# Performance work log

Measured on AMD Instinct MI355X. Metric: run time of the kernel, lower is better.

The kernel has to match this reference:

```python
import jax, jax.numpy as jnp
import numpy as np

N = 50000   # nodes
E = 800000  # edges
K = 3       # hops per TAGConv


def _row_normalize(x):
    row_sum = jnp.clip(jnp.sum(x, axis=1, keepdims=True), 1e-8, None)
    return x / row_sum


def _gcn_norm(edge_index, num_nodes):
    # PyG gcn_norm with add_self_loops=False (TAGConv default), edge_weight=1
    src, dst = edge_index[0], edge_index[1]
    deg = jax.ops.segment_sum(jnp.ones((src.shape[0],), jnp.float32), dst,
                              num_segments=num_nodes)
    deg_inv_sqrt = jnp.where(deg > 0, jnp.where(deg > 0, deg, 1.0) ** -0.5, 0.0)
    return deg_inv_sqrt[src] * deg_inv_sqrt[dst]  # [E]


def _propagate(x, src, dst, norm, num_nodes):
    # out[dst] += norm * x[src]   (sparse sym-normalized SpMM)
    return jax.ops.segment_sum(norm[:, None] * x[src], dst, num_segments=num_nodes)


def _tagconv(x, edge_index, norm, W, b):
    # W: [K+1, d_in, d_out]; out = sum_k A_hat^k x @ W_k + b
    src, dst = edge_index[0], edge_index[1]
    n = x.shape[0]
    hops = [x]
    for _ in range(W.shape[0] - 1):
        hops.append(_propagate(hops[-1], src, dst, norm, n))
    H = jnp.stack(hops)  # [K+1, N, d_in]
    return jnp.einsum('knd,kdo->no', H, W) + b


def setup_inputs() -> dict:
    key = jax.random.key(0)
    k1, k2, k3, k4 = jax.random.split(key, 4)
    x = jax.random.normal(k1, (N, 128), jnp.float32)
    edge_index = jax.random.randint(k2, (2, E), 0, N, jnp.int32)
    W1 = jax.random.normal(k3, (K + 1, 128, 16), jnp.float32) * 0.1
    b1 = jnp.zeros((16,), jnp.float32)
    W2 = jax.random.normal(k4, (K + 1, 16, 64), jnp.float32) * 0.1
    b2 = jnp.zeros((64,), jnp.float32)
    return {"x": x, "edge_index": edge_index, "W1": W1, "b1": b1,
            "W2": W2, "b2": b2}


def reference(x, edge_index, W1, b1, W2, b2):
    n = x.shape[0]
    norm = _gcn_norm(edge_index, n)
    h = _row_normalize(x)
    h = jax.nn.relu(_tagconv(h, edge_index, norm, W1, b1))
    # dropout is identity in eval mode
    return _tagconv(h, edge_index, norm, W2, b2)
```

## Files before the change

kernel.cpp:

```cpp
#include <hip/hip_runtime.h>
#include <hip/hip_bf16.h>

typedef unsigned short u16;

__device__ __forceinline__ float bf2f(u16 h) {
    return __uint_as_float(((unsigned int)h) << 16);
}
__device__ __forceinline__ u16 f2bf(float f) {
    __hip_bfloat16 h = __float2bfloat16(f);
    return *reinterpret_cast<u16*>(&h);
}

__global__ void pos_kernel(const int* __restrict__ dst, int* __restrict__ cnt,
                           int* __restrict__ pos, int E) {
    int e = blockIdx.x * blockDim.x + threadIdx.x;
    if (e < E) pos[e] = atomicAdd(&cnt[dst[e]], 1);
}

__global__ __launch_bounds__(256) void scanA_kernel(const int* __restrict__ cnt,
                                                    int* __restrict__ rowptr,
                                                    int* __restrict__ bsum, int n) {
    __shared__ int lds[256];
    int i = blockIdx.x * 256 + threadIdx.x;
    int v = (i < n) ? cnt[i] : 0;
    lds[threadIdx.x] = v;
    __syncthreads();
    #pragma unroll
    for (int off = 1; off < 256; off <<= 1) {
        int t = (threadIdx.x >= off) ? lds[threadIdx.x - off] : 0;
        __syncthreads();
        lds[threadIdx.x] += t;
        __syncthreads();
    }
    if (i < n) rowptr[i + 1] = lds[threadIdx.x];
    if (threadIdx.x == 255) bsum[blockIdx.x] = lds[255];
}

__global__ __launch_bounds__(1024) void scanB_kernel(int* __restrict__ bsum, int nb) {
    __shared__ int lds[1024];
    int t = threadIdx.x;
    int v = (t < nb) ? bsum[t] : 0;
    lds[t] = v;
    __syncthreads();
    #pragma unroll
    for (int off = 1; off < 1024; off <<= 1) {
        int u = (t >= off) ? lds[t - off] : 0;
        __syncthreads();
        lds[t] += u;
        __syncthreads();
    }
    if (t < nb) bsum[t] = lds[t] - v;
}

__global__ __launch_bounds__(256) void scanC_dis_kernel(int* __restrict__ rowptr,
                                                        const int* __restrict__ bsum,
                                                        const int* __restrict__ cnt,
                                                        float* __restrict__ dis, int n) {
    int i = blockIdx.x * 256 + threadIdx.x;
    if (i < n) {
        rowptr[i + 1] += bsum[blockIdx.x];
        int d = cnt[i];
        dis[i] = (d > 0) ? rsqrtf((float)d) : 0.0f;
    }
    if (i == 0) rowptr[0] = 0;
}

__global__ __launch_bounds__(1024) void scan_kernel(const int* __restrict__ cnt,
                                                    int* __restrict__ rowptr, int n) {
    __shared__ int part[1024];
    int tid = threadIdx.x;
    int chunk = (n + 1023) / 1024;
    int beg = tid * chunk;
    int end = beg + chunk; if (end > n) end = n;
    int s = 0;
    for (int i = beg; i < end; ++i) s += cnt[i];
    part[tid] = s;
    __syncthreads();
    for (int off = 1; off < 1024; off <<= 1) {
        int v = (tid >= off) ? part[tid - off] : 0;
        __syncthreads();
        part[tid] += v;
        __syncthreads();
    }
    int run = (tid > 0) ? part[tid - 1] : 0;
    if (tid == 0) rowptr[0] = 0;
    for (int i = beg; i < end; ++i) { run += cnt[i]; rowptr[i + 1] = run; }
}

__global__ void dis_only_kernel(const int* __restrict__ cnt, float* __restrict__ dis, int n) {
    int i = blockIdx.x * blockDim.x + threadIdx.x;
    if (i < n) {
        int d = cnt[i];
        dis[i] = (d > 0) ? rsqrtf((float)d) : 0.0f;
    }
}

__global__ void scatter2_kernel(const int* __restrict__ src, const int* __restrict__ dst,
                                const int* __restrict__ pos, const float* __restrict__ dis,
                                const int* __restrict__ rowptr,
                                float2* __restrict__ ecolw, int E) {
    int e = blockIdx.x * blockDim.x + threadIdx.x;
    if (e < E) {
        int s = src[e], d = dst[e];
        ecolw[rowptr[d] + pos[e]] = make_float2(__int_as_float(s), dis[s] * dis[d]);
    }
}

__global__ __launch_bounds__(256) void gemm1_bf_kernel(
    const float* __restrict__ x, const float* __restrict__ W1,
    u16* __restrict__ zb, int n, int nstride)
{
    __shared__ float As[64 * 132];
    __shared__ float Bs[64 * 64];
    __shared__ float sums[128];
    const int t  = threadIdx.x;
    const int tx = t & 15;
    const int ty = t >> 4;
    const int c  = t & 15;
    const int g  = t >> 4;
    const int block_row = blockIdx.x * 128;

    float acc[8][4];
    #pragma unroll
    for (int i = 0; i < 8; ++i)
        #pragma unroll
        for (int j = 0; j < 4; ++j) acc[i][j] = 0.f;

    for (int kp = 0; kp < 2; ++kp) {
        #pragma unroll
        for (int i = 0; i < 8; ++i) {
            int row  = g + 16 * i;
            int grow = block_row + row;
            float v0 = 0.f, v1 = 0.f, v2 = 0.f, v3 = 0.f;
            if (grow < n) {
                const float* xp = x + (long)grow * 128 + kp * 64 + c;
                v0 = xp[0]; v1 = xp[16]; v2 = xp[32]; v3 = xp[48];
            }
            As[(c +  0) * 132 + row] = v0;
            As[(c + 16) * 132 + row] = v1;
            As[(c + 32) * 132 + row] = v2;
            As[(c + 48) * 132 + row] = v3;
            float red = (v0 + v1) + (v2 + v3);
            #pragma unroll
            for (int off = 8; off > 0; off >>= 1) red += __shfl_down(red, off, 16);
            if (c == 0) { if (kp == 0) sums[row] = red; else sums[row] += red; }
        }
        #pragma unroll
        for (int i2 = 0; i2 < 4; ++i2) {
            int kk = g + 16 * i2;
            int kglob = kp * 64 + kk;
            float4 wv = *(const float4*)(W1 + (c >> 2) * 2048 + kglob * 16 + 4 * (c & 3));
            *(float4*)(Bs + kk * 64 + 4 * c) = wv;
        }
        __syncthreads();
        #pragma unroll 4
        for (int kk = 0; kk < 64; ++kk) {
            float4 a0 = *(const float4*)(As + kk * 132 + 8 * ty);
            float4 a1 = *(const float4*)(As + kk * 132 + 8 * ty + 4);
            float4 bv = *(const float4*)(Bs + kk * 64 + 4 * tx);
            float ar[8] = {a0.x, a0.y, a0.z, a0.w, a1.x, a1.y, a1.z, a1.w};
            float br[4] = {bv.x, bv.y, bv.z, bv.w};
            #pragma unroll
            for (int i = 0; i < 8; ++i)
                #pragma unroll
                for (int j = 0; j < 4; ++j)
                    acc[i][j] += ar[i] * br[j];
        }
        __syncthreads();
    }
    int plane = tx >> 2;
    int oo4   = 4 * (tx & 3);
    #pragma unroll
    for (int i = 0; i < 8; ++i) {
        int row  = 8 * ty + i;
        int grow = block_row + row;
        if (grow < n) {
            float s = 1.0f / fmaxf(sums[row], 1e-8f);
            ushort4 o;
            o.x = f2bf(acc[i][0] * s); o.y = f2bf(acc[i][1] * s);
            o.z = f2bf(acc[i][2] * s); o.w = f2bf(acc[i][3] * s);
            *(ushort4*)(zb + (long)plane * nstride + (long)grow * 16 + oo4) = o;
        }
    }
}

__global__ __launch_bounds__(256) void spmm_csr_bf_kernel(
    const u16* __restrict__ in, const u16* __restrict__ addsrc,
    u16* __restrict__ out, const int* __restrict__ rowptr,
    const float2* __restrict__ ecolw, const float* __restrict__ b,
    int relu, int n)
{
    int t = blockIdx.x * blockDim.x + threadIdx.x;
    int r = t >> 2, q = t & 3;
    if (r >= n) return;
    int e0 = rowptr[r], e1 = rowptr[r + 1];
    float a0x=0,a0y=0,a0z=0,a0w=0, a1x=0,a1y=0,a1z=0,a1w=0;
    float a2x=0,a2y=0,a2z=0,a2w=0, a3x=0,a3y=0,a3z=0,a3w=0;
    int e = e0;
    for (; e + 4 <= e1; e += 4) {
        float2 c0 = ecolw[e], c1 = ecolw[e+1], c2 = ecolw[e+2], c3 = ecolw[e+3];
        ushort4 v0 = *((const ushort4*)(in + (long)__float_as_int(c0.x) * 16) + q);
        ushort4 v1 = *((const ushort4*)(in + (long)__float_as_int(c1.x) * 16) + q);
        ushort4 v2 = *((const ushort4*)(in + (long)__float_as_int(c2.x) * 16) + q);
        ushort4 v3 = *((const ushort4*)(in + (long)__float_as_int(c3.x) * 16) + q);
        a0x += c0.y * bf2f(v0.x); a0y += c0.y * bf2f(v0.y); a0z += c0.y * bf2f(v0.z); a0w += c0.y * bf2f(v0.w);
        a1x += c1.y * bf2f(v1.x); a1y += c1.y * bf2f(v1.y); a1z += c1.y * bf2f(v1.z); a1w += c1.y * bf2f(v1.w);
        a2x += c2.y * bf2f(v2.x); a2y += c2.y * bf2f(v2.y); a2z += c2.y * bf2f(v2.z); a2w += c2.y * bf2f(v2.w);
        a3x += c3.y * bf2f(v3.x); a3y += c3.y * bf2f(v3.y); a3z += c3.y * bf2f(v3.z); a3w += c3.y * bf2f(v3.w);
    }
    for (; e < e1; ++e) {
        float2 c0 = ecolw[e];
        ushort4 v0 = *((const ushort4*)(in + (long)__float_as_int(c0.x) * 16) + q);
        a0x += c0.y * bf2f(v0.x); a0y += c0.y * bf2f(v0.y); a0z += c0.y * bf2f(v0.z); a0w += c0.y * bf2f(v0.w);
    }
    float Ax = (a0x+a1x)+(a2x+a3x), Ay = (a0y+a1y)+(a2y+a3y);
    float Az = (a0z+a1z)+(a2z+a3z), Aw = (a0w+a1w)+(a2w+a3w);
    if (addsrc) {
        ushort4 s = *((const ushort4*)(addsrc + (long)r * 16) + q);
        Ax += bf2f(s.x); Ay += bf2f(s.y); Az += bf2f(s.z); Aw += bf2f(s.w);
    }
    if (b) {
        float4 bb = *((const float4*)b + q);
        Ax += bb.x; Ay += bb.y; Az += bb.z; Aw += bb.w;
    }
    if (relu) {
        Ax = fmaxf(Ax, 0.f); Ay = fmaxf(Ay, 0.f);
        Az = fmaxf(Az, 0.f); Aw = fmaxf(Aw, 0.f);
    }
    ushort4 o; o.x = f2bf(Ax); o.y = f2bf(Ay); o.z = f2bf(Az); o.w = f2bf(Aw);
    *((ushort4*)(out + (long)r * 16) + q) = o;
}

__global__ __launch_bounds__(256) void gemm2_bf_kernel(
    const u16* __restrict__ zb, const float* __restrict__ W2,
    const float* __restrict__ b2, float* __restrict__ out, int n, int nstride)
{
    __shared__ float As[64 * 132];
    __shared__ float Bs[64 * 64];
    const int t  = threadIdx.x;
    const int tx = t & 15;
    const int ty = t >> 4;
    const int c  = t & 15;
    const int g  = t >> 4;
    const int block_row = blockIdx.x * 128;

    float acc[8][4];
    #pragma unroll
    for (int i = 0; i < 8; ++i)
        #pragma unroll
        for (int j = 0; j < 4; ++j) acc[i][j] = 0.f;

    #pragma unroll
    for (int i = 0; i < 8; ++i) {
        int row  = g + 16 * i;
        int grow = block_row + row;
        float v0 = 0.f, v1 = 0.f, v2 = 0.f, v3 = 0.f;
        if (grow < n) {
            const u16* zp = zb + (long)grow * 16 + c;
            v0 = bf2f(zp[0]);
            v1 = bf2f(zp[(long)nstride]);
            v2 = bf2f(zp[2 * (long)nstride]);
            v3 = bf2f(zp[3 * (long)nstride]);
        }
        As[(c +  0) * 132 + row] = v0;
        As[(c + 16) * 132 + row] = v1;
        As[(c + 32) * 132 + row] = v2;
        As[(c + 48) * 132 + row] = v3;
    }
    #pragma unroll
    for (int i2 = 0; i2 < 4; ++i2) {
        int j = g + 16 * i2;
        float4 wv = *(const float4*)(W2 + j * 64 + 4 * c);
        *(float4*)(Bs + j * 64 + 4 * c) = wv;
    }
    __syncthreads();
    #pragma unroll 4
    for (int kk = 0; kk < 64; ++kk) {
        float4 a0 = *(const float4*)(As + kk * 132 + 8 * ty);
        float4 a1 = *(const float4*)(As + kk * 132 + 8 * ty + 4);
        float4 bv = *(const float4*)(Bs + kk * 64 + 4 * tx);
        float ar[8] = {a0.x, a0.y, a0.z, a0.w, a1.x, a1.y, a1.z, a1.w};
        float br[4] = {bv.x, bv.y, bv.z, bv.w};
        #pragma unroll
        for (int i = 0; i < 8; ++i)
            #pragma unroll
            for (int j = 0; j < 4; ++j)
                acc[i][j] += ar[i] * br[j];
    }
    float4 bias = *(const float4*)(b2 + 4 * tx);
    #pragma unroll
    for (int i = 0; i < 8; ++i) {
        int grow = block_row + 8 * ty + i;
        if (grow < n) {
            float4 o = make_float4(acc[i][0] + bias.x, acc[i][1] + bias.y,
                                   acc[i][2] + bias.z, acc[i][3] + bias.w);
            *(float4*)(out + (long)grow * 64 + 4 * tx) = o;
        }
    }
}

__global__ void deg_kernel(const int* __restrict__ dst, float* __restrict__ deg, int E) {
    int e = blockIdx.x * blockDim.x + threadIdx.x;
    if (e < E) atomicAdd(&deg[dst[e]], 1.0f);
}
__global__ void disf_kernel(float* __restrict__ deg, int n) {
    int i = blockIdx.x * blockDim.x + threadIdx.x;
    if (i < n) {
        float d = deg[i];
        deg[i] = (d > 0.0f) ? rsqrtf(d) : 0.0f;
    }
}
__global__ __launch_bounds__(256) void gemm1_f32_kernel(
    const float* __restrict__ x, const float* __restrict__ W1,
    float* __restrict__ z, int n, int nstride)
{
    __shared__ float As[64 * 132];
    __shared__ float Bs[64 * 64];
    __shared__ float sums[128];
    const int t  = threadIdx.x;
    const int tx = t & 15;
    const int ty = t >> 4;
    const int c  = t & 15;
    const int g  = t >> 4;
    const int block_row = blockIdx.x * 128;
    float acc[8][4];
    #pragma unroll
    for (int i = 0; i < 8; ++i)
        #pragma unroll
        for (int j = 0; j < 4; ++j) acc[i][j] = 0.f;
    for (int kp = 0; kp < 2; ++kp) {
        #pragma unroll
        for (int i = 0; i < 8; ++i) {
            int row  = g + 16 * i;
            int grow = block_row + row;
            float v0 = 0.f, v1 = 0.f, v2 = 0.f, v3 = 0.f;
            if (grow < n) {
                const float* xp = x + (long)grow * 128 + kp * 64 + c;
                v0 = xp[0]; v1 = xp[16]; v2 = xp[32]; v3 = xp[48];
            }
            As[(c +  0) * 132 + row] = v0;
            As[(c + 16) * 132 + row] = v1;
            As[(c + 32) * 132 + row] = v2;
            As[(c + 48) * 132 + row] = v3;
            float red = (v0 + v1) + (v2 + v3);
            #pragma unroll
            for (int off = 8; off > 0; off >>= 1) red += __shfl_down(red, off, 16);
            if (c == 0) { if (kp == 0) sums[row] = red; else sums[row] += red; }
        }
        #pragma unroll
        for (int i2 = 0; i2 < 4; ++i2) {
            int kk = g + 16 * i2;
            int kglob = kp * 64 + kk;
            float4 wv = *(const float4*)(W1 + (c >> 2) * 2048 + kglob * 16 + 4 * (c & 3));
            *(float4*)(Bs + kk * 64 + 4 * c) = wv;
        }
        __syncthreads();
        #pragma unroll 4
        for (int kk = 0; kk < 64; ++kk) {
            float4 a0 = *(const float4*)(As + kk * 132 + 8 * ty);
            float4 a1 = *(const float4*)(As + kk * 132 + 8 * ty + 4);
            float4 bv = *(const float4*)(Bs + kk * 64 + 4 * tx);
            float ar[8] = {a0.x, a0.y, a0.z, a0.w, a1.x, a1.y, a1.z, a1.w};
            float br[4] = {bv.x, bv.y, bv.z, bv.w};
            #pragma unroll
            for (int i = 0; i < 8; ++i)
                #pragma unroll
                for (int j = 0; j < 4; ++j)
                    acc[i][j] += ar[i] * br[j];
        }
        __syncthreads();
    }
    int plane = tx >> 2;
    int oo4   = 4 * (tx & 3);
    #pragma unroll
    for (int i = 0; i < 8; ++i) {
        int row  = 8 * ty + i;
        int grow = block_row + row;
        if (grow < n) {
            float s = 1.0f / fmaxf(sums[row], 1e-8f);
            float4 o = make_float4(acc[i][0] * s, acc[i][1] * s, acc[i][2] * s, acc[i][3] * s);
            *(float4*)(z + (long)plane * nstride + (long)grow * 16 + oo4) = o;
        }
    }
}
__global__ __launch_bounds__(256) void spmm_atomic_kernel(
    const float* __restrict__ in, float* __restrict__ out,
    const int* __restrict__ src, const int* __restrict__ dst,
    const float* __restrict__ dis, int E)
{
    int t = blockIdx.x * blockDim.x + threadIdx.x;
    int e = t >> 4, f = t & 15;
    if (e < E) {
        int s = src[e], d = dst[e];
        atomicAdd(&out[d * 16 + f], dis[s] * dis[d] * in[s * 16 + f]);
    }
}
__global__ void bias_relu_kernel(float* __restrict__ z0, const float* __restrict__ b, int total) {
    int i = blockIdx.x * blockDim.x + threadIdx.x;
    if (i < total) {
        float v = z0[i] + b[i & 15];
        z0[i] = v > 0.0f ? v : 0.0f;
    }
}
__global__ __launch_bounds__(256) void gemm2_f32_kernel(
    const float* __restrict__ z, const float* __restrict__ W2,
    const float* __restrict__ b2, float* __restrict__ out, int n, int nstride)
{
    __shared__ float As[64 * 132];
    __shared__ float Bs[64 * 64];
    const int t  = threadIdx.x;
    const int tx = t & 15;
    const int ty = t >> 4;
    const int c  = t & 15;
    const int g  = t >> 4;
    const int block_row = blockIdx.x * 128;
    float acc[8][4];
    #pragma unroll
    for (int i = 0; i < 8; ++i)
        #pragma unroll
        for (int j = 0; j < 4; ++j) acc[i][j] = 0.f;
    #pragma unroll
    for (int i = 0; i < 8; ++i) {
        int row  = g + 16 * i;
        int grow = block_row + row;
        float v0 = 0.f, v1 = 0.f, v2 = 0.f, v3 = 0.f;
        if (grow < n) {
            const float* zp = z + (long)grow * 16 + c;
            v0 = zp[0];
            v1 = zp[(long)nstride];
            v2 = zp[2 * (long)nstride];
            v3 = zp[3 * (long)nstride];
        }
        As[(c +  0) * 132 + row] = v0;
        As[(c + 16) * 132 + row] = v1;
        As[(c + 32) * 132 + row] = v2;
        As[(c + 48) * 132 + row] = v3;
    }
    #pragma unroll
    for (int i2 = 0; i2 < 4; ++i2) {
        int j = g + 16 * i2;
        float4 wv = *(const float4*)(W2 + j * 64 + 4 * c);
        *(float4*)(Bs + j * 64 + 4 * c) = wv;
    }
    __syncthreads();
    #pragma unroll 4
    for (int kk = 0; kk < 64; ++kk) {
        float4 a0 = *(const float4*)(As + kk * 132 + 8 * ty);
        float4 a1 = *(const float4*)(As + kk * 132 + 8 * ty + 4);
        float4 bv = *(const float4*)(Bs + kk * 64 + 4 * tx);
        float ar[8] = {a0.x, a0.y, a0.z, a0.w, a1.x, a1.y, a1.z, a1.w};
        float br[4] = {bv.x, bv.y, bv.z, bv.w};
        #pragma unroll
        for (int i = 0; i < 8; ++i)
            #pragma unroll
            for (int j = 0; j < 4; ++j)
                acc[i][j] += ar[i] * br[j];
    }
    float4 bias = *(const float4*)(b2 + 4 * tx);
    #pragma unroll
    for (int i = 0; i < 8; ++i) {
        int grow = block_row + 8 * ty + i;
        if (grow < n) {
            float4 o = make_float4(acc[i][0] + bias.x, acc[i][1] + bias.y,
                                   acc[i][2] + bias.z, acc[i][3] + bias.w);
            *(float4*)(out + (long)grow * 64 + 4 * tx) = o;
        }
    }
}

static inline size_t align16(size_t v) { return (v + 15) & ~(size_t)15; }

extern "C" void kernel_launch(void* const* d_in, const int* in_sizes, int n_in,
                              void* d_out, int out_size, void* d_ws, size_t ws_size,
                              hipStream_t stream) {
    const float* x   = (const float*)d_in[0];
    const int*   ei  = (const int*)d_in[1];
    const float* W1  = (const float*)d_in[2];
    const float* b1  = (const float*)d_in[3];
    const float* W2  = (const float*)d_in[4];
    const float* bb2 = (const float*)d_in[5];
    float* out = (float*)d_out;

    const int n  = in_sizes[0] / 128;
    const int E  = in_sizes[1] / 2;
    const int NS = n * 16;

    const int* srcp = ei;
    const int* dstp = ei + E;

    char* wsb = (char*)d_ws;
    int*   cnt    = (int*)wsb;
    int*   rowptr = (int*)(wsb + (size_t)4 * n);
    int*   bsum   = (int*)(wsb + (size_t)4 * (2 * n + 1));
    float* dis    = (float*)(wsb + (size_t)4 * (2 * n + 1 + 1024));
    size_t zoffb  = align16((size_t)4 * (3 * n + 1 + 1024));
    u16*   zb     = (u16*)(wsb + zoffb);
    size_t posoff = align16(zoffb + (size_t)2 * 4 * NS);
    int*   pos    = (int*)(wsb + posoff);
    size_t ecooff = align16(posoff + (size_t)4 * E);
    float2* ecolw = (float2*)(wsb + ecooff);
    size_t need   = ecooff + (size_t)8 * E;

    int gemm_blocks = (n + 127) / 128;

    if (ws_size >= need) {
        int nb = (n + 255) / 256;
        hipMemsetAsync(cnt, 0, (size_t)n * sizeof(int), stream);
        pos_kernel<<<(E + 255) / 256, 256, 0, stream>>>(dstp, cnt, pos, E);
        if (nb <= 1024) {
            scanA_kernel<<<nb, 256, 0, stream>>>(cnt, rowptr, bsum, n);
            scanB_kernel<<<1, 1024, 0, stream>>>(bsum, nb);
            scanC_dis_kernel<<<nb, 256, 0, stream>>>(rowptr, bsum, cnt, dis, n);
        } else {
            scan_kernel<<<1, 1024, 0, stream>>>(cnt, rowptr, n);
            dis_only_kernel<<<(n + 255) / 256, 256, 0, stream>>>(cnt, dis, n);
        }
        scatter2_kernel<<<(E + 255) / 256, 256, 0, stream>>>(srcp, dstp, pos, dis, rowptr, ecolw, E);

        gemm1_bf_kernel<<<gemm_blocks, 256, 0, stream>>>(x, W1, zb, n, NS);

        int sb = (4 * n + 255) / 256;
        spmm_csr_bf_kernel<<<sb, 256, 0, stream>>>(zb + 3 * NS, zb + 2 * NS, zb + 2 * NS, rowptr, ecolw, nullptr, 0, n);
        spmm_csr_bf_kernel<<<sb, 256, 0, stream>>>(zb + 2 * NS, zb + 1 * NS, zb + 1 * NS, rowptr, ecolw, nullptr, 0, n);
        spmm_csr_bf_kernel<<<sb, 256, 0, stream>>>(zb + 1 * NS, zb,          zb,          rowptr, ecolw, b1,      1, n);
        spmm_csr_bf_kernel<<<sb, 256, 0, stream>>>(zb,          nullptr, zb + 1 * NS, rowptr, ecolw, nullptr, 0, n);
        spmm_csr_bf_kernel<<<sb, 256, 0, stream>>>(zb + 1 * NS, nullptr, zb + 2 * NS, rowptr, ecolw, nullptr, 0, n);
        spmm_csr_bf_kernel<<<sb, 256, 0, stream>>>(zb + 2 * NS, nullptr, zb + 3 * NS, rowptr, ecolw, nullptr, 0, n);

        gemm2_bf_kernel<<<gemm_blocks, 256, 0, stream>>>(zb, W2, bb2, out, n, NS);
    } else {
        float* ws = (float*)d_ws;
        float* dis2 = ws;
        size_t z2off = ((size_t)n + 3) & ~(size_t)3;
        float* z2 = ws + z2off;
        hipMemsetAsync(dis2, 0, n * sizeof(float), stream);
        deg_kernel<<<(E + 255) / 256, 256, 0, stream>>>(dstp, dis2, E);
        disf_kernel<<<(n + 255) / 256, 256, 0, stream>>>(dis2, n);
        gemm1_f32_kernel<<<gemm_blocks, 256, 0, stream>>>(x, W1, z2, n, NS);
        int sb = (16 * E + 255) / 256;
        spmm_atomic_kernel<<<sb, 256, 0, stream>>>(z2 + 3 * NS, z2 + 2 * NS, srcp, dstp, dis2, E);
        spmm_atomic_kernel<<<sb, 256, 0, stream>>>(z2 + 2 * NS, z2 + 1 * NS, srcp, dstp, dis2, E);
        spmm_atomic_kernel<<<sb, 256, 0, stream>>>(z2 + 1 * NS, z2,          srcp, dstp, dis2, E);
        bias_relu_kernel<<<(NS + 255) / 256, 256, 0, stream>>>(z2, b1, NS);
        hipMemsetAsync(z2 + NS, 0, (size_t)3 * NS * sizeof(float), stream);
        spmm_atomic_kernel<<<sb, 256, 0, stream>>>(z2,          z2 + NS,     srcp, dstp, dis2, E);
        spmm_atomic_kernel<<<sb, 256, 0, stream>>>(z2 + NS,     z2 + 2 * NS, srcp, dstp, dis2, E);
        spmm_atomic_kernel<<<sb, 256, 0, stream>>>(z2 + 2 * NS, z2 + 3 * NS, srcp, dstp, dis2, E);
        gemm2_f32_kernel<<<gemm_blocks, 256, 0, stream>>>(z2, W2, bb2, out, n, NS);
    }
}
```

Before: 239.9 us.

## Build CSR via bucketed two-pass sort with LDS histograms instead of global atomics

Replaces the old CSR construction with a bucket sort on destination node (128 nodes per bucket). The old path used one global atomic per edge on per-node counters, then a scan and a random scatter. The new path builds per-chunk bucket histograms in LDS, scans them, scatters (src,dst) pairs into buckets, then finalizes each bucket in one block: local degree count, rowptr, degree-norm and CSR fill. A separate pass then multiplies in the source-side normalization. The aim is to remove contended global atomics and improve write locality, at the cost of more kernel launches and an extra 8-byte-per-edge intermediate buffer. The serial per-bucket prefix loop in the finalize kernel, and a scan branch that is skipped when the scan needs more than 1024 blocks, are possible weak points.

```diff
diff --git a/kernel.cpp b/kernel.cpp
--- a/kernel.cpp
+++ b/kernel.cpp
@@ -11,18 +11,31 @@
     return *reinterpret_cast<u16*>(&h);
 }
 
-__global__ void pos_kernel(const int* __restrict__ dst, int* __restrict__ cnt,
-                           int* __restrict__ pos, int E) {
-    int e = blockIdx.x * blockDim.x + threadIdx.x;
-    if (e < E) pos[e] = atomicAdd(&cnt[dst[e]], 1);
-}
-
-__global__ __launch_bounds__(256) void scanA_kernel(const int* __restrict__ cnt,
-                                                    int* __restrict__ rowptr,
+#define BKT_SHIFT 7
+#define BKT_SIZE  128
+#define CHUNK     2048
+
+__global__ __launch_bounds__(256) void hist_kernel(const int* __restrict__ dst,
+                                                   int* __restrict__ hist,
+                                                   int E, int nbA, int nbuck) {
+    __shared__ int lh[512];
+    for (int j = threadIdx.x; j < nbuck; j += 256) lh[j] = 0;
+    __syncthreads();
+    int base = blockIdx.x * CHUNK;
+    int end  = min(E, base + CHUNK);
+    for (int e = base + threadIdx.x; e < end; e += 256)
+        atomicAdd(&lh[dst[e] >> BKT_SHIFT], 1);
+    __syncthreads();
+    for (int j = threadIdx.x; j < nbuck; j += 256)
+        hist[j * nbA + blockIdx.x] = lh[j];
+}
+
+__global__ __launch_bounds__(256) void scanA_kernel(const int* __restrict__ in,
+                                                    int* __restrict__ outp1,
                                                     int* __restrict__ bsum, int n) {
     __shared__ int lds[256];
     int i = blockIdx.x * 256 + threadIdx.x;
-    int v = (i < n) ? cnt[i] : 0;
+    int v = (i < n) ? in[i] : 0;
     lds[threadIdx.x] = v;
     __syncthreads();
     #pragma unroll
@@ -32,10 +45,9 @@
         lds[threadIdx.x] += t;
         __syncthreads();
     }
-    if (i < n) rowptr[i + 1] = lds[threadIdx.x];
+    if (i < n) outp1[i + 1] = lds[threadIdx.x];
     if (threadIdx.x == 255) bsum[blockIdx.x] = lds[255];
 }
-
 __global__ __launch_bounds__(1024) void scanB_kernel(int* __restrict__ bsum, int nb) {
     __shared__ int lds[1024];
     int t = threadIdx.x;
@@ -51,58 +63,86 @@
     }
     if (t < nb) bsum[t] = lds[t] - v;
 }
-
-__global__ __launch_bounds__(256) void scanC_dis_kernel(int* __restrict__ rowptr,
-                                                        const int* __restrict__ bsum,
-                                                        const int* __restrict__ cnt,
-                                                        float* __restrict__ dis, int n) {
+__global__ __launch_bounds__(256) void scanC_kernel(int* __restrict__ outp1,
+                                                    const int* __restrict__ bsum, int n) {
     int i = blockIdx.x * 256 + threadIdx.x;
-    if (i < n) {
-        rowptr[i + 1] += bsum[blockIdx.x];
-        int d = cnt[i];
-        dis[i] = (d > 0) ? rsqrtf((float)d) : 0.0f;
-    }
-    if (i == 0) rowptr[0] = 0;
-}
-
-__global__ __launch_bounds__(1024) void scan_kernel(const int* __restrict__ cnt,
-                                                    int* __restrict__ rowptr, int n) {
-    __shared__ int part[1024];
-    int tid = threadIdx.x;
-    int chunk = (n + 1023) / 1024;
-    int beg = tid * chunk;
-    int end = beg + chunk; if (end > n) end = n;
-    int s = 0;
-    for (int i = beg; i < end; ++i) s += cnt[i];
-    part[tid] = s;
-    __syncthreads();
-    for (int off = 1; off < 1024; off <<= 1) {
-        int v = (tid >= off) ? part[tid - off] : 0;
-        __syncthreads();
-        part[tid] += v;
-        __syncthreads();
-    }
-    int run = (tid > 0) ? part[tid - 1] : 0;
-    if (tid == 0) rowptr[0] = 0;
-    for (int i = beg; i < end; ++i) { run += cnt[i]; rowptr[i + 1] = run; }
-}
-
-__global__ void dis_only_kernel(const int* __restrict__ cnt, float* __restrict__ dis, int n) {
-    int i = blockIdx.x * blockDim.x + threadIdx.x;
-    if (i < n) {
-        int d = cnt[i];
-        dis[i] = (d > 0) ? rsqrtf((float)d) : 0.0f;
-    }
-}
-
-__global__ void scatter2_kernel(const int* __restrict__ src, const int* __restrict__ dst,
-                                const int* __restrict__ pos, const float* __restrict__ dis,
-                                const int* __restrict__ rowptr,
-                                float2* __restrict__ ecolw, int E) {
+    if (i < n) outp1[i + 1] += bsum[blockIdx.x];
+    if (i == 0) outp1[0] = 0;
+}
+
+__global__ __launch_bounds__(256) void bucket_scatter_kernel(
+    const int* __restrict__ src, const int* __restrict__ dst,
+    const int* __restrict__ hofs, int2* __restrict__ bucketed,
+    int E, int nbA, int nbuck)
+{
+    __shared__ int lbase[512];
+    __shared__ int lcnt[512];
+    for (int j = threadIdx.x; j < nbuck; j += 256) {
+        lbase[j] = hofs[j * nbA + blockIdx.x];
+        lcnt[j] = 0;
+    }
+    __syncthreads();
+    int base = blockIdx.x * CHUNK;
+    int end  = min(E, base + CHUNK);
+    for (int e = base + threadIdx.x; e < end; e += 256) {
+        int d = dst[e];
+        int b = d >> BKT_SHIFT;
+        int r = atomicAdd(&lcnt[b], 1);
+        bucketed[lbase[b] + r] = make_int2(src[e], d);
+    }
+}
+
+__global__ __launch_bounds__(256) void csr_finalize_kernel(
+    const int2* __restrict__ bucketed, const int* __restrict__ hofs,
+    int* __restrict__ rowptr, float* __restrict__ dis,
+    float2* __restrict__ ecolw, int E, int nbA, int nbuck, int n)
+{
+    __shared__ int cnt[BKT_SIZE];
+    __shared__ int run[BKT_SIZE];
+    __shared__ float disl[BKT_SIZE];
+    int b = blockIdx.x;
+    int bstart = hofs[b * nbA];
+    int bend   = (b == nbuck - 1) ? E : hofs[(b + 1) * nbA];
+    for (int j = threadIdx.x; j < BKT_SIZE; j += 256) cnt[j] = 0;
+    __syncthreads();
+    for (int i = bstart + threadIdx.x; i < bend; i += 256)
+        atomicAdd(&cnt[bucketed[i].y & (BKT_SIZE - 1)], 1);
+    __syncthreads();
+    if (threadIdx.x == 0) {
+        int runacc = 0;
+        for (int j = 0; j < BKT_SIZE; ++j) {
+            int c = cnt[j];
+            run[j] = runacc;
+            runacc += c;
+        }
+    }
+    __syncthreads();
+    for (int j = threadIdx.x; j < BKT_SIZE; j += 256) {
+        int d = b * BKT_SIZE + j;
+        if (d < n) {
+            rowptr[d] = bstart + run[j];
+            int c = cnt[j];
+            float dv = (c > 0) ? rsqrtf((float)c) : 0.0f;
+            dis[d] = dv;
+            disl[j] = dv;
+        }
+    }
+    if (b == 0 && threadIdx.x == 0) rowptr[n] = E;
+    __syncthreads();
+    for (int i = bstart + threadIdx.x; i < bend; i += 256) {
+        int2 p = bucketed[i];
+        int j = p.y & (BKT_SIZE - 1);
+        int r = atomicAdd(&run[j], 1);
+        ecolw[bstart + r] = make_float2(__int_as_float(p.x), disl[j]);
+    }
+}
+
+__global__ __launch_bounds__(256) void weight_kernel(float2* __restrict__ ecolw,
+                                                     const float* __restrict__ dis, int E) {
     int e = blockIdx.x * blockDim.x + threadIdx.x;
     if (e < E) {
-        int s = src[e], d = dst[e];
-        ecolw[rowptr[d] + pos[e]] = make_float2(__int_as_float(s), dis[s] * dis[d]);
+        float2 c = ecolw[e];
+        ecolw[e].y = c.y * dis[__float_as_int(c.x)];
     }
 }
 
@@ -488,34 +528,37 @@
     const int* srcp = ei;
     const int* dstp = ei + E;
 
+    const int nbuck = (n + BKT_SIZE - 1) >> BKT_SHIFT;
+    const int nbA   = (E + CHUNK - 1) / CHUNK;
+    const int m     = nbuck * nbA;
+    const int nbS   = (m + 255) / 256;
+
     char* wsb = (char*)d_ws;
-    int*   cnt    = (int*)wsb;
-    int*   rowptr = (int*)(wsb + (size_t)4 * n);
-    int*   bsum   = (int*)(wsb + (size_t)4 * (2 * n + 1));
-    float* dis    = (float*)(wsb + (size_t)4 * (2 * n + 1 + 1024));
-    size_t zoffb  = align16((size_t)4 * (3 * n + 1 + 1024));
+    int*   hist   = (int*)wsb;
+    int*   hofs   = (int*)(wsb + (size_t)4 * m);
+    int*   bsum   = (int*)(wsb + (size_t)4 * (2 * m + 1));
+    int*   rowptr = (int*)(wsb + (size_t)4 * (2 * m + 1 + 1024));
+    float* dis    = (float*)(wsb + (size_t)4 * (2 * m + 1 + 1024 + n + 1));
+    size_t zoffb  = align16((size_t)4 * (2 * m + 1 + 1024 + 2 * n + 1));
     u16*   zb     = (u16*)(wsb + zoffb);
-    size_t posoff = align16(zoffb + (size_t)2 * 4 * NS);
-    int*   pos    = (int*)(wsb + posoff);
-    size_t ecooff = align16(posoff + (size_t)4 * E);
+    size_t bkoff  = align16(zoffb + (size_t)2 * 4 * NS);
+    int2*  bucketed = (int2*)(wsb + bkoff);
+    size_t ecooff = align16(bkoff + (size_t)8 * E);
     float2* ecolw = (float2*)(wsb + ecooff);
     size_t need   = ecooff + (size_t)8 * E;
 
     int gemm_blocks = (n + 127) / 128;
 
-    if (ws_size >= need) {
-        int nb = (n + 255) / 256;
-        hipMemsetAsync(cnt, 0, (size_t)n * sizeof(int), stream);
-        pos_kernel<<<(E + 255) / 256, 256, 0, stream>>>(dstp, cnt, pos, E);
-        if (nb <= 1024) {
-            scanA_kernel<<<nb, 256, 0, stream>>>(cnt, rowptr, bsum, n);
-            scanB_kernel<<<1, 1024, 0, stream>>>(bsum, nb);
-            scanC_dis_kernel<<<nb, 256, 0, stream>>>(rowptr, bsum, cnt, dis, n);
-        } else {
-            scan_kernel<<<1, 1024, 0, stream>>>(cnt, rowptr, n);
-            dis_only_kernel<<<(n + 255) / 256, 256, 0, stream>>>(cnt, dis, n);
-        }
-        scatter2_kernel<<<(E + 255) / 256, 256, 0, stream>>>(srcp, dstp, pos, dis, rowptr, ecolw, E);
+    if (ws_size >= need && nbuck <= 512 && nbS <= 256 * 1024) {
+        hist_kernel<<<nbA, 256, 0, stream>>>(dstp, hist, E, nbA, nbuck);
+        if (nbS <= 1024) {
+            scanA_kernel<<<nbS, 256, 0, stream>>>(hist, hofs, bsum, m);
+            scanB_kernel<<<1, 1024, 0, stream>>>(bsum, nbS);
+            scanC_kernel<<<nbS, 256, 0, stream>>>(hofs, bsum, m);
+        }
+        bucket_scatter_kernel<<<nbA, 256, 0, stream>>>(srcp, dstp, hofs, bucketed, E, nbA, nbuck);
+        csr_finalize_kernel<<<nbuck, 256, 0, stream>>>(bucketed, hofs, rowptr, dis, ecolw, E, nbA, nbuck, n);
+        weight_kernel<<<(E + 255) / 256, 256, 0, stream>>>(ecolw, dis, E);
 
         gemm1_bf_kernel<<<gemm_blocks, 256, 0, stream>>>(x, W1, zb, n, NS);
 
```

Result: faster. 214.7 us (-10.5%).
